# Kernel optimization log

Measured on AMD Instinct MI355X. Metric: run time of the kernel, lower is better.

## Reference

```python
import jax, jax.numpy as jnp
from jax import lax
import numpy as np

EXPLORED_MAP = 1  # MC.EXPLORED_MAP channel index


def _disk(radius: int) -> np.ndarray:
    # skimage.morphology.disk(radius): Euclidean disk structuring element
    y, x = np.ogrid[-radius:radius + 1, -radius:radius + 1]
    return (x * x + y * y <= radius * radius).astype(np.float32)


def setup_inputs() -> dict:
    key = jax.random.key(0)
    B, C, M = 8, 24, 960  # (batch, 8 + num_sem_categories, map, map)
    # explored-map channel is binary {0,1}; other channels arbitrary
    map_features = jax.random.randint(key, (B, C, M, M), 0, 2).astype(jnp.float32)
    dilate_explored_kernel = jnp.asarray(_disk(10))[None, None]  # (1,1,21,21)
    select_border_kernel = jnp.asarray(_disk(1))[None, None]     # (1,1,3,3)
    return {
        "map_features": map_features,
        "dilate_explored_kernel": dilate_explored_kernel,
        "select_border_kernel": select_border_kernel,
    }


def _conv_same(x, k):
    # x: (B,1,M,M), k: (1,1,kh,kw); SAME padding, stride 1
    return lax.conv_general_dilated(
        x, k, window_strides=(1, 1), padding="SAME",
        dimension_numbers=("NCHW", "OIHW", "NCHW"))


def binary_erosion(x, k):
    return jnp.clip(_conv_same(x, k) - jnp.sum(k) + 1.0, 0.0, 1.0)


def binary_dilation(x, k):
    return jnp.clip(_conv_same(x, k), 0.0, 1.0)


def reference(map_features, dilate_explored_kernel, select_border_kernel):
    # frontier = unexplored cells
    frontier = (map_features[:, EXPLORED_MAP:EXPLORED_MAP + 1] == 0).astype(map_features.dtype)
    eroded = binary_erosion(frontier, dilate_explored_kernel)
    goal_map = binary_dilation(eroded, select_border_kernel) - eroded  # border of eroded frontier
    return goal_map  # (B, 1, M, M)
```

## Files before the change

### kernel.cpp

```cpp
#include <hip/hip_runtime.h>
#include <stdint.h>


#define MDIM 960
#define NW 15
#define TILE 8
#define RSTAGE (TILE + 22)
#define EROWS (TILE + 2)
#define NTHREADS 256
#define NBATCH 8
#define NCHAN 24
#define EXPLORED_CH 1
#define ROWS_TOTAL (NBATCH * MDIM)
#define PACK_BLOCKS 480

__global__ __launch_bounds__(NTHREADS) void frontier_pack_kernel(
    const float* __restrict__ in, uint64_t* __restrict__ ws)
{
    const int wave = blockIdx.x * (NTHREADS / 64) + (threadIdx.x >> 6);
    const int lane = threadIdx.x & 63;
    #pragma unroll
    for (int rr = 0; rr < 4; ++rr) {
        const int R = wave * 4 + rr;
        const int b = R / MDIM, row = R % MDIM;
        const float* src = in + ((size_t)b * NCHAN + EXPLORED_CH) * MDIM * MDIM
                              + (size_t)row * MDIM;
        uint64_t w[NW];
        #pragma unroll
        for (int j = 0; j < NW; ++j) {
            float v = src[j * 64 + lane];
            w[j] = __ballot(v == 0.0f);
        }
        if (lane == 0) {
            uint64_t* dst = ws + (size_t)R * NW;
            #pragma unroll
            for (int j = 0; j < NW; ++j) dst[j] = w[j];
        }
    }
}

__global__ __launch_bounds__(NTHREADS) void frontier_morph_kernel(
    const uint64_t* __restrict__ ws, float* __restrict__ out)
{
    __shared__ uint64_t sF[RSTAGE][NW];
    __shared__ uint64_t sH[6][RSTAGE][NW];
    __shared__ uint64_t sE[EROWS][NW];

    const int bx   = blockIdx.x;
    const int b    = bx / (MDIM / TILE);
    const int tile = bx % (MDIM / TILE);
    const int i0   = tile * TILE;
    const int tid  = threadIdx.x;

    const uint64_t* pk = ws + (size_t)b * MDIM * NW;
    for (int t = tid; t < RSTAGE * NW; t += NTHREADS) {
        int l = t / NW, wd = t % NW;
        int g = i0 - 11 + l;
        sF[l][wd] = (g >= 0 && g < MDIM) ? pk[(size_t)g * NW + wd] : 0ull;
    }
    __syncthreads();

    for (int t = tid; t < RSTAGE * NW; t += NTHREADS) {
        int l = t / NW, wd = t % NW;
        uint64_t a  = (wd > 0)      ? sF[l][wd - 1] : 0ull;
        uint64_t bb = sF[l][wd];
        uint64_t c  = (wd < NW - 1) ? sF[l][wd + 1] : 0ull;
        #pragma unroll
        for (int k = 1; k <= 10; ++k) {
            uint64_t da = (a >> 1) | (bb << 63);
            uint64_t db = (bb >> 1) | (c << 63);
            uint64_t dc = (c >> 1);
            uint64_t ua = (a << 1);
            uint64_t ub = (bb << 1) | (a >> 63);
            uint64_t uc = (c << 1) | (bb >> 63);
            a  &= da & ua;
            bb &= db & ub;
            c  &= dc & uc;
            if (k == 4)  sH[0][l][wd] = bb;
            if (k == 6)  sH[1][l][wd] = bb;
            if (k == 7)  sH[2][l][wd] = bb;
            if (k == 8)  sH[3][l][wd] = bb;
            if (k == 9)  sH[4][l][wd] = bb;
            if (k == 10) sH[5][l][wd] = bb;
        }
    }
    __syncthreads();

    for (int t = tid; t < EROWS * NW; t += NTHREADS) {
        int r = t / NW, wd = t % NW;
        uint64_t e = sF[r][wd] & sF[r + 20][wd];
        e &= sH[0][r + 1][wd] & sH[0][r + 19][wd];
        e &= sH[1][r + 2][wd] & sH[1][r + 18][wd];
        e &= sH[2][r + 3][wd] & sH[2][r + 17][wd];
        e &= sH[3][r + 4][wd] & sH[3][r + 16][wd];
        e &= sH[3][r + 5][wd] & sH[3][r + 15][wd];
        e &= sH[4][r + 6][wd] & sH[4][r + 14][wd];
        e &= sH[4][r + 7][wd] & sH[4][r + 13][wd];
        e &= sH[4][r + 8][wd] & sH[4][r + 12][wd];
        e &= sH[4][r + 9][wd] & sH[4][r + 11][wd];
        e &= sH[5][r + 10][wd];
        sE[r][wd] = e;
    }
    __syncthreads();

    float* dst = out + (size_t)b * MDIM * MDIM;
    for (int t = tid; t < TILE * (MDIM / 4); t += NTHREADS) {
        int ro = t / (MDIM / 4), c4 = t % (MDIM / 4);
        int c0 = c4 * 4;
        float vj[4];
        #pragma unroll
        for (int j = 0; j < 4; ++j) {
            int col = c0 + j;
            int wd = col >> 6, sh = col & 63;
            unsigned e  = (unsigned)((sE[ro + 1][wd] >> sh) & 1);
            unsigned n  = (unsigned)((sE[ro    ][wd] >> sh) & 1);
            unsigned s  = (unsigned)((sE[ro + 2][wd] >> sh) & 1);
            unsigned lf = (col > 0)
                ? (unsigned)((sE[ro + 1][(col - 1) >> 6] >> ((col - 1) & 63)) & 1) : 0u;
            unsigned rt = (col < MDIM - 1)
                ? (unsigned)((sE[ro + 1][(col + 1) >> 6] >> ((col + 1) & 63)) & 1) : 0u;
            unsigned d = e | n | s | lf | rt;
            vj[j] = (float)(d & (e ^ 1u));
        }
        float4 v = make_float4(vj[0], vj[1], vj[2], vj[3]);
        *(float4*)(dst + (size_t)(i0 + ro) * MDIM + c0) = v;
    }
}

extern "C" void kernel_launch(void* const* d_in, const int* in_sizes, int n_in,
                              void* d_out, int out_size, void* d_ws, size_t ws_size,
                              hipStream_t stream)
{
    const float* mapf = (const float*)d_in[0];
    float* out = (float*)d_out;
    uint64_t* ws = (uint64_t*)d_ws;

    frontier_pack_kernel<<<dim3(PACK_BLOCKS), NTHREADS, 0, stream>>>(mapf, ws);
    frontier_morph_kernel<<<dim3(NBATCH * (MDIM / TILE)), NTHREADS, 0, stream>>>(ws, out);
}
```

Measured before the change: 754.0 us.

## Double morph tile height and compute horizontal erosions by doubling shifts

Raises the row tile from 8 to 16, so each block's 22-row halo is amortized over more output rows and the grid holds half as many blocks. It also replaces the ten unit-shift horizontal erosion steps with eight steps, two of which shift by 2 (erosion run-length doubling). Both aim to cut redundant halo loads and the ALU work of the horizontal stage. The cost is more shared memory per block and fewer blocks in flight.

```diff
diff --git a/kernel.cpp b/kernel.cpp
--- a/kernel.cpp
+++ b/kernel.cpp
@@ -4,14 +4,13 @@
 
 #define MDIM 960
 #define NW 15
-#define TILE 8
+#define TILE 16
 #define RSTAGE (TILE + 22)
 #define EROWS (TILE + 2)
 #define NTHREADS 256
 #define NBATCH 8
 #define NCHAN 24
 #define EXPLORED_CH 1
-#define ROWS_TOTAL (NBATCH * MDIM)
 #define PACK_BLOCKS 480
 
 __global__ __launch_bounds__(NTHREADS) void frontier_pack_kernel(
@@ -37,6 +36,20 @@
             for (int j = 0; j < NW; ++j) dst[j] = w[j];
         }
     }
+}
+
+template<int K>
+__device__ __forceinline__ void erode3(uint64_t& a, uint64_t& b, uint64_t& c)
+{
+    uint64_t da = (a >> K) | (b << (64 - K));
+    uint64_t db = (b >> K) | (c << (64 - K));
+    uint64_t dc = (c >> K);
+    uint64_t ua = (a << K);
+    uint64_t ub = (b << K) | (a >> (64 - K));
+    uint64_t uc = (c << K) | (b >> (64 - K));
+    a &= da & ua;
+    b &= db & ub;
+    c &= dc & uc;
 }
 
 __global__ __launch_bounds__(NTHREADS) void frontier_morph_kernel(
@@ -65,24 +78,14 @@
         uint64_t a  = (wd > 0)      ? sF[l][wd - 1] : 0ull;
         uint64_t bb = sF[l][wd];
         uint64_t c  = (wd < NW - 1) ? sF[l][wd + 1] : 0ull;
-        #pragma unroll
-        for (int k = 1; k <= 10; ++k) {
-            uint64_t da = (a >> 1) | (bb << 63);
-            uint64_t db = (bb >> 1) | (c << 63);
-            uint64_t dc = (c >> 1);
-            uint64_t ua = (a << 1);
-            uint64_t ub = (bb << 1) | (a >> 63);
-            uint64_t uc = (c << 1) | (bb >> 63);
-            a  &= da & ua;
-            bb &= db & ub;
-            c  &= dc & uc;
-            if (k == 4)  sH[0][l][wd] = bb;
-            if (k == 6)  sH[1][l][wd] = bb;
-            if (k == 7)  sH[2][l][wd] = bb;
-            if (k == 8)  sH[3][l][wd] = bb;
-            if (k == 9)  sH[4][l][wd] = bb;
-            if (k == 10) sH[5][l][wd] = bb;
-        }
+        erode3<1>(a, bb, c);
+        erode3<1>(a, bb, c);
+        erode3<2>(a, bb, c); sH[0][l][wd] = bb;
+        erode3<2>(a, bb, c); sH[1][l][wd] = bb;
+        erode3<1>(a, bb, c); sH[2][l][wd] = bb;
+        erode3<1>(a, bb, c); sH[3][l][wd] = bb;
+        erode3<1>(a, bb, c); sH[4][l][wd] = bb;
+        erode3<1>(a, bb, c); sH[5][l][wd] = bb;
     }
     __syncthreads();
 
```

After: 758.1 us. About the same (+0.5%).
